# Performance work log

Hardware: AMD Instinct MI355X
Metric: run time of the kernel (lower is better)

## Reference

```python
import jax, jax.numpy as jnp
import numpy as np

B, S, HID = 1, 4096, 2048
H, HKV, D = 16, 4, 128
BLOCK = 32          # dllm_block_length
EPS = 1e-6
SCALE = D ** -0.5


def setup_inputs() -> dict:
    key = jax.random.key(0)
    ks = jax.random.split(key, 4)
    hidden_states = jax.random.normal(ks[0], (B, S, HID), dtype=jnp.float32)
    # RoPE tables (interleaved-half convention), shape [S, D]
    inv_freq = 1.0 / (10000.0 ** (np.arange(0, D, 2, dtype=np.float32) / D))
    t = np.arange(S, dtype=np.float32)
    freqs = np.outer(t, inv_freq)                      # [S, D/2]
    emb = np.concatenate([freqs, freqs], axis=-1)      # [S, D]
    cos = jnp.asarray(np.cos(emb), dtype=jnp.float32)
    sin = jnp.asarray(np.sin(emb), dtype=jnp.float32)
    w_qkv = jax.random.normal(ks[1], (HID, (H + 2 * HKV) * D), dtype=jnp.float32) * (HID ** -0.5)
    w_o = jax.random.normal(ks[2], (H * D, HID), dtype=jnp.float32) * ((H * D) ** -0.5)
    q_norm_w = jnp.ones((D,), dtype=jnp.float32)
    k_norm_w = jnp.ones((D,), dtype=jnp.float32)
    return {"hidden_states": hidden_states, "cos": cos, "sin": sin,
            "w_qkv": w_qkv, "q_norm_w": q_norm_w, "k_norm_w": k_norm_w, "w_o": w_o}


def _rms_norm(x, w):
    var = jnp.mean(jnp.square(x), axis=-1, keepdims=True)
    return x * jax.lax.rsqrt(var + EPS) * w


def _rotate_half(x):
    x1, x2 = jnp.split(x, 2, axis=-1)
    return jnp.concatenate([-x2, x1], axis=-1)


def reference(hidden_states, cos, sin, w_qkv, q_norm_w, k_norm_w, w_o):
    b, s, _ = hidden_states.shape
    qkv = hidden_states @ w_qkv                                   # [B,S,(H+2Hkv)*D]
    q = qkv[..., : H * D].reshape(b, s, H, D)
    k = qkv[..., H * D: (H + HKV) * D].reshape(b, s, HKV, D)
    v = qkv[..., (H + HKV) * D:].reshape(b, s, HKV, D)
    # per-head RMSNorm on q/k (use_qk_norm)
    q = _rms_norm(q, q_norm_w)
    k = _rms_norm(k, k_norm_w)
    # RoPE
    c = cos[None, :, None, :]
    sn = sin[None, :, None, :]
    q = q * c + _rotate_half(q) * sn
    k = k * c + _rotate_half(k) * sn
    # GQA: repeat kv heads
    rep = H // HKV
    k = jnp.repeat(k, rep, axis=2)                                # [B,S,H,D]
    v = jnp.repeat(v, rep, axis=2)
    scores = jnp.einsum("bshd,bthd->bhst", q, k) * SCALE          # [B,H,S,S]
    # block-diffusion mask: bidirectional within a dllm block, causal across blocks
    blk = jnp.arange(s) // BLOCK
    allowed = blk[None, :] <= blk[:, None]                        # [S,S]
    scores = jnp.where(allowed[None, None], scores, jnp.finfo(scores.dtype).min)
    attn = jax.nn.softmax(scores, axis=-1)
    out = jnp.einsum("bhst,bthd->bshd", attn, v).reshape(b, s, H * D)
    return out @ w_o
```

## Files before the change

kernel.cpp:

```cpp
#include <hip/hip_runtime.h>
#include <cstdint>

typedef __bf16 bf16;
typedef __attribute__((ext_vector_type(4))) __bf16 bf16x4;
typedef __attribute__((ext_vector_type(8))) __bf16 bf16x8;
typedef __attribute__((ext_vector_type(4))) float f32x4;

#define MFMA16(a, b, c) __builtin_amdgcn_mfma_f32_16x16x32_bf16((a), (b), (c), 0, 0, 0)

static __device__ __forceinline__ void gload16(const void* g, void* l) {
  __builtin_amdgcn_global_load_lds(
      (const __attribute__((address_space(1))) void*)g,
      (__attribute__((address_space(3))) void*)l, 16, 0, 0);
}

#define SWZ128(r, k) ((r) * 128 + ((k) ^ (((r) & 7) << 3)))
#define SWZP(r, k)   ((r) * 64  + ((k) ^ (((r) & 7) << 3)))
#define SWZV(r, k)   ((r) * 64  + ((k) ^ (((r) & 7) << 3)))

__global__ __launch_bounds__(256) void k_convert(const float* __restrict__ in,
                                                 bf16* __restrict__ out, int n4) {
  int i = blockIdx.x * blockDim.x + threadIdx.x;
  if (i >= n4) return;
  float4 v = *(const float4*)&in[(size_t)i * 4];
  bf16x4 o;
  o[0] = (bf16)v.x; o[1] = (bf16)v.y; o[2] = (bf16)v.z; o[3] = (bf16)v.w;
  *(bf16x4*)&out[(size_t)i * 4] = o;
}

__global__ void k_transpose(const float* __restrict__ in, bf16* __restrict__ out,
                            int R, int C) {
  __shared__ float tile[32][33];
  int bx = blockIdx.x, by = blockIdx.y;
  int tx = threadIdx.x, ty = threadIdx.y;
#pragma unroll
  for (int i = ty; i < 32; i += 8)
    tile[i][tx] = in[(size_t)(by * 32 + i) * C + bx * 32 + tx];
  __syncthreads();
#pragma unroll
  for (int i = ty; i < 32; i += 8)
    out[(size_t)(bx * 32 + i) * R + by * 32 + tx] = (bf16)tile[tx][i];
}

__global__ void k_vtrans(const bf16* __restrict__ qkv, bf16* __restrict__ vtg) {
  __shared__ bf16 tile[32][33];
  int s0 = blockIdx.x * 32, d0 = blockIdx.y * 32, hk = blockIdx.z;
  int tx = threadIdx.x, ty = threadIdx.y;
#pragma unroll
  for (int i = ty; i < 32; i += 8)
    tile[i][tx] = qkv[(size_t)(s0 + i) * 3072 + 2560 + hk * 128 + d0 + tx];
  __syncthreads();
#pragma unroll
  for (int i = ty; i < 32; i += 8)
    vtg[(size_t)hk * 524288 + (size_t)(d0 + i) * 4096 + s0 + tx] = tile[tx][i];
}

template <typename OutT>
__global__ __launch_bounds__(256) void k_gemm(const bf16* __restrict__ A,
                                              const bf16* __restrict__ BT,
                                              OutT* __restrict__ C, int M, int N, int K) {
  __shared__ bf16 As[128 * 32];
  __shared__ bf16 Bs[128 * 32];
  const int tid = threadIdx.x;
  const int wv = tid >> 6, lane = tid & 63;
  const int lr = lane & 15, lg = lane >> 4;
  const int wm = (wv >> 1) * 64, wn = (wv & 1) * 64;
  const int bm = blockIdx.x, bn = blockIdx.y;
  const size_t baseA = (size_t)bm * 128 * K;
  const size_t baseB = (size_t)bn * 128 * K;
  f32x4 acc[4][4] = {};
  for (int kt = 0; kt < K; kt += 32) {
    __syncthreads();
#pragma unroll
    for (int inst = 0; inst < 2; ++inst) {
      int ch = inst * 256 + tid;
      int row = ch >> 2, ko = (ch & 3) * 8;
      gload16(A + baseA + (size_t)row * K + kt + ko, &As[(size_t)(inst * 256 + wv * 64) * 8]);
      gload16(BT + baseB + (size_t)row * K + kt + ko, &Bs[(size_t)(inst * 256 + wv * 64) * 8]);
    }
    __syncthreads();
    bf16x8 af[4], bfr[4];
#pragma unroll
    for (int mi = 0; mi < 4; ++mi) af[mi] = *(const bf16x8*)&As[(wm + mi * 16 + lr) * 32 + lg * 8];
#pragma unroll
    for (int nj = 0; nj < 4; ++nj) bfr[nj] = *(const bf16x8*)&Bs[(wn + nj * 16 + lr) * 32 + lg * 8];
#pragma unroll
    for (int mi = 0; mi < 4; ++mi)
#pragma unroll
      for (int nj = 0; nj < 4; ++nj)
        acc[mi][nj] = MFMA16(af[mi], bfr[nj], acc[mi][nj]);
  }
#pragma unroll
  for (int mi = 0; mi < 4; ++mi)
#pragma unroll
    for (int nj = 0; nj < 4; ++nj)
#pragma unroll
      for (int j = 0; j < 4; ++j) {
        int r = bm * 128 + wm + mi * 16 + lg * 4 + j;
        int c = bn * 128 + wn + nj * 16 + lr;
        C[(size_t)r * N + c] = (OutT)acc[mi][nj][j];
      }
}

__global__ __launch_bounds__(256) void k_rmsrope(bf16* __restrict__ qkv,
                                                 const float* __restrict__ cosb,
                                                 const float* __restrict__ sinb,
                                                 const float* __restrict__ qw,
                                                 const float* __restrict__ kw) {
  int row = blockIdx.x * 4 + (threadIdx.x >> 6);
  int lane = threadIdx.x & 63;
  int s = row / 20, hd = row % 20;
  bool isq = hd < 16;
  int col = isq ? hd * 128 : 2048 + (hd - 16) * 128;
  bf16* p = qkv + (size_t)s * 3072 + col;
  float x1 = (float)p[lane], x2 = (float)p[lane + 64];
  float ss = x1 * x1 + x2 * x2;
#pragma unroll
  for (int m = 32; m; m >>= 1) ss += __shfl_xor(ss, m);
  float r = rsqrtf(ss * (1.0f / 128.0f) + 1e-6f);
  const float* w = isq ? qw : kw;
  float y1 = x1 * r * w[lane], y2 = x2 * r * w[lane + 64];
  float c1 = cosb[s * 128 + lane], c2 = cosb[s * 128 + lane + 64];
  float s1 = sinb[s * 128 + lane], s2 = sinb[s * 128 + lane + 64];
  p[lane] = (bf16)(y1 * c1 - y2 * s1);
  p[lane + 64] = (bf16)(y2 * c2 + y1 * s2);
}

__global__ __launch_bounds__(512, 2) void k_attn(const bf16* __restrict__ qkv,
                                                 const bf16* __restrict__ vtg,
                                                 bf16* __restrict__ out,
                                                 bf16* __restrict__ pO,
                                                 float2* __restrict__ pml) {
  __shared__ bf16 Ks[64 * 128];
  __shared__ bf16 Pl[128 * 64];
  __shared__ bf16 Vt[128 * 64];
  const int tid = threadIdx.x;
  const int wv = tid >> 6, lane = tid & 63;
  const int lr = lane & 15, lg = lane >> 4;
  const int b = blockIdx.x;
  int h, qt, kb0, kb1, tile = 0, half = 0;
  bool split;
  if (b < 256) {
    h = b & 15; qt = b >> 4; kb0 = 0; kb1 = 2 * qt + 2; split = false;
  } else {
    half = (b >= 512);
    int u = b - (half ? 512 : 256);
    h = u & 15; qt = 31 - (u >> 4);
    tile = h * 16 + (qt - 16);
    const int nh = qt + 1;
    kb0 = half ? nh : 0;
    kb1 = half ? 2 * qt + 2 : nh;
    split = true;
  }
  const int q0 = qt * 128;
  const int hk = h >> 2;
  const int wq = wv * 16;
  const float K2 = 0.12751744f;

  const int chK0 = tid, chK1 = 512 + tid;
  const int rowK0 = chK0 >> 4, rowK1 = chK1 >> 4;
  const int doffK0 = ((chK0 & 15) * 8) ^ ((rowK0 & 7) << 3);
  const int doffK1 = ((chK1 & 15) * 8) ^ ((rowK1 & 7) << 3);
  const int drow0 = chK0 >> 3, drow1 = chK1 >> 3;
  const int koffV0 = ((chK0 & 7) * 8) ^ ((drow0 & 7) << 3);
  const int koffV1 = ((chK1 & 7) * 8) ^ ((drow1 & 7) << 3);
  const bf16* kp0 = qkv + 2048 + hk * 128 + doffK0 + (size_t)(kb0 * 64 + rowK0) * 3072;
  const bf16* kp1 = qkv + 2048 + hk * 128 + doffK1 + (size_t)(kb0 * 64 + rowK1) * 3072;
  const bf16* vp0 = vtg + (size_t)hk * 524288 + (size_t)drow0 * 4096 + koffV0 + kb0 * 64;
  const bf16* vp1 = vtg + (size_t)hk * 524288 + (size_t)drow1 * 4096 + koffV1 + kb0 * 64;

  bf16x8 qf[4];
  {
    const bf16* qrow = qkv + (size_t)(q0 + wq + lr) * 3072 + h * 128 + lg * 8;
#pragma unroll
    for (int kk = 0; kk < 4; ++kk) {
      bf16x8 v = *(const bf16x8*)(qrow + kk * 32);
#pragma unroll
      for (int i = 0; i < 8; ++i) v[i] = (bf16)((float)v[i] * K2);
      qf[kk] = v;
    }
  }

  f32x4 oacc[8] = {};
  float mst = -1e30f, lst = 0.f;
  const int lim = (wq + lr) | 31;

  for (int kb = kb0; kb < kb1; ++kb) {
    __syncthreads();
    gload16(kp0, &Ks[(size_t)(wv * 64) * 8]);
    gload16(kp1, &Ks[(size_t)(512 + wv * 64) * 8]);
    gload16(vp0, &Vt[(size_t)(wv * 64) * 8]);
    gload16(vp1, &Vt[(size_t)(512 + wv * 64) * 8]);
    kp0 += 64 * 3072; kp1 += 64 * 3072; vp0 += 64; vp1 += 64;
    __syncthreads();

    f32x4 sacc[4] = {};
#pragma unroll
    for (int kk = 0; kk < 4; ++kk) {
      bf16x8 bk[4];
#pragma unroll
      for (int a = 0; a < 4; ++a)
        bk[a] = *(const bf16x8*)&Ks[SWZ128(a * 16 + lr, kk * 32 + lg * 8)];
#pragma unroll
      for (int a = 0; a < 4; ++a)
        sacc[a] = MFMA16(bk[a], qf[kk], sacc[a]);
    }

    float rm = -1e30f;
    if (kb >= 2 * qt) {
      const int koff2 = (kb - 2 * qt) * 64;
#pragma unroll
      for (int a = 0; a < 4; ++a)
#pragma unroll
        for (int j = 0; j < 4; ++j) {
          float sv = sacc[a][j];
          if (koff2 + a * 16 + lg * 4 + j > lim) sv = -1e30f;
          sacc[a][j] = sv;
          rm = fmaxf(rm, sv);
        }
    } else {
#pragma unroll
      for (int a = 0; a < 4; ++a)
#pragma unroll
        for (int j = 0; j < 4; ++j) rm = fmaxf(rm, sacc[a][j]);
    }
    rm = fmaxf(rm, __shfl_xor(rm, 16));
    rm = fmaxf(rm, __shfl_xor(rm, 32));
    if (__any(rm - mst > 8.0f)) {
      float mnew = fmaxf(mst, rm);
      float al = exp2f(mst - mnew);
      mst = mnew;
      lst *= al;
      float alo[4];
#pragma unroll
      for (int j = 0; j < 4; ++j) alo[j] = __shfl(al, lg * 4 + j);
#pragma unroll
      for (int dj = 0; dj < 8; ++dj)
#pragma unroll
        for (int j = 0; j < 4; ++j) oacc[dj][j] *= alo[j];
    }
    float rs = 0.f;
#pragma unroll
    for (int a = 0; a < 4; ++a) {
      bf16x4 pw;
#pragma unroll
      for (int j = 0; j < 4; ++j) {
        float p = exp2f(sacc[a][j] - mst);
        rs += p;
        pw[j] = (bf16)p;
      }
      *(bf16x4*)&Pl[SWZP(wq + lr, a * 16 + lg * 4)] = pw;
    }
    rs += __shfl_xor(rs, 16);
    rs += __shfl_xor(rs, 32);
    lst += rs;

#pragma unroll
    for (int kk = 0; kk < 2; ++kk) {
      bf16x8 ap = *(const bf16x8*)&Pl[SWZP(wq + lr, kk * 32 + lg * 8)];
#pragma unroll
      for (int dj = 0; dj < 8; ++dj) {
        bf16x8 bv = *(const bf16x8*)&Vt[SWZV(dj * 16 + lr, kk * 32 + lg * 8)];
        oacc[dj] = MFMA16(ap, bv, oacc[dj]);
      }
    }
  }

  float lrec = 1.0f / lst;
  float linv[4];
#pragma unroll
  for (int j = 0; j < 4; ++j) linv[j] = __shfl(lrec, lg * 4 + j);
  if (!split) {
#pragma unroll
    for (int dj = 0; dj < 8; ++dj)
#pragma unroll
      for (int j = 0; j < 4; ++j) {
        int srow = q0 + wq + lg * 4 + j;
        int d = dj * 16 + lr;
        out[(size_t)srow * 2048 + h * 128 + d] = (bf16)(oacc[dj][j] * linv[j]);
      }
  } else {
    if (lg == 0) pml[((size_t)half * 256 + tile) * 128 + wq + lr] = make_float2(mst, lst);
    bf16* pb = pO + (((size_t)half * 256 + tile) * 128) * 128;
#pragma unroll
    for (int dj = 0; dj < 8; ++dj)
#pragma unroll
      for (int j = 0; j < 4; ++j) {
        int row = wq + lg * 4 + j;
        int d = dj * 16 + lr;
        pb[(size_t)row * 128 + d] = (bf16)(oacc[dj][j] * linv[j]);
      }
  }
}

__global__ __launch_bounds__(256) void k_comb(const bf16* __restrict__ pO,
                                              const float2* __restrict__ pml,
                                              bf16* __restrict__ attno) {
  const int tile = blockIdx.x;
  const int h = tile >> 4, qt = 16 + (tile & 15);
  const int t = threadIdx.x;
  const int r = blockIdx.y * 32 + (t >> 3);
  const int d0 = (t & 7) * 16;
  float2 m0 = pml[(size_t)tile * 128 + r];
  float2 m1 = pml[(size_t)(256 + tile) * 128 + r];
  float mm = fmaxf(m0.x, m1.x);
  float w0 = m0.y * exp2f(m0.x - mm);
  float w1 = m1.y * exp2f(m1.x - mm);
  float inv = 1.0f / (w0 + w1);
  w0 *= inv; w1 *= inv;
  const bf16* p0 = pO + ((size_t)tile * 128 + r) * 128 + d0;
  const bf16* p1 = pO + ((size_t)(256 + tile) * 128 + r) * 128 + d0;
  bf16* o = attno + (size_t)(qt * 128 + r) * 2048 + h * 128 + d0;
#pragma unroll
  for (int v = 0; v < 2; ++v) {
    bf16x8 a = *(const bf16x8*)(p0 + v * 8);
    bf16x8 c = *(const bf16x8*)(p1 + v * 8);
    bf16x8 ov;
#pragma unroll
    for (int i = 0; i < 8; ++i) ov[i] = (bf16)((float)a[i] * w0 + (float)c[i] * w1);
    *(bf16x8*)(o + v * 8) = ov;
  }
}

extern "C" void kernel_launch(void* const* d_in, const int* in_sizes, int n_in,
                              void* d_out, int out_size, void* d_ws, size_t ws_size,
                              hipStream_t stream) {
  const float* hs = (const float*)d_in[0];
  const float* cosb = (const float*)d_in[1];
  const float* sinb = (const float*)d_in[2];
  const float* w_qkv = (const float*)d_in[3];
  const float* qw = (const float*)d_in[4];
  const float* kw = (const float*)d_in[5];
  const float* w_o = (const float*)d_in[6];
  float* out = (float*)d_out;

  char* ws = (char*)d_ws;
  bf16* qkv   = (bf16*)(ws);
  bf16* hsb   = (bf16*)(ws + 25165824);
  bf16* wqkvT = (bf16*)(ws + 41943040);
  bf16* woT   = (bf16*)(ws + 41943040);
  bf16* attno = (bf16*)(ws + 25165824);
  bf16* vtg   = (bf16*)(ws + 54525952);
  bf16* pO    = (bf16*)(ws + 58720256);
  float2* pml = (float2*)(ws + 75497472);

  k_convert<<<8192, 256, 0, stream>>>(hs, hsb, 2097152);
  k_transpose<<<dim3(96, 64), dim3(32, 8), 0, stream>>>(w_qkv, wqkvT, 2048, 3072);
  k_gemm<bf16><<<dim3(32, 24), 256, 0, stream>>>(hsb, wqkvT, qkv, 4096, 3072, 2048);
  k_rmsrope<<<20480, 256, 0, stream>>>(qkv, cosb, sinb, qw, kw);
  k_vtrans<<<dim3(128, 4, 4), dim3(32, 8), 0, stream>>>(qkv, vtg);
  k_transpose<<<dim3(64, 64), dim3(32, 8), 0, stream>>>(w_o, woT, 2048, 2048);
  k_attn<<<768, 512, 0, stream>>>(qkv, vtg, attno, pO, pml);
  k_comb<<<dim3(256, 4), 256, 0, stream>>>(pO, pml, attno);
  k_gemm<float><<<dim3(32, 16), 256, 0, stream>>>(attno, woT, out, 4096, 2048, 2048);
}
```

Before: 292.3 us.

## Fuse per-head RMSNorm and RoPE into the QKV projection GEMM epilogue

Replaces the generic QKV GEMM plus separate RMSNorm/RoPE kernel with a dedicated GEMM whose 128-column tile equals one head. Warps now own full 128-wide rows, so the epilogue can reduce the sum of squares with lane shuffles, apply the norm weight and rotate-half RoPE, then write bf16 directly. This removes one kernel launch and a full read and write of the q/k activations. In exchange the tile shape changes to 32x128 per warp with 16 accumulators, and the epilogue issues scattered scalar cos/sin loads and stores, which may change register pressure and GEMM efficiency.

```diff
diff --git a/kernel.cpp b/kernel.cpp
--- a/kernel.cpp
+++ b/kernel.cpp
@@ -102,28 +102,89 @@
       }
 }
 
-__global__ __launch_bounds__(256) void k_rmsrope(bf16* __restrict__ qkv,
-                                                 const float* __restrict__ cosb,
-                                                 const float* __restrict__ sinb,
-                                                 const float* __restrict__ qw,
-                                                 const float* __restrict__ kw) {
-  int row = blockIdx.x * 4 + (threadIdx.x >> 6);
-  int lane = threadIdx.x & 63;
-  int s = row / 20, hd = row % 20;
-  bool isq = hd < 16;
-  int col = isq ? hd * 128 : 2048 + (hd - 16) * 128;
-  bf16* p = qkv + (size_t)s * 3072 + col;
-  float x1 = (float)p[lane], x2 = (float)p[lane + 64];
-  float ss = x1 * x1 + x2 * x2;
-#pragma unroll
-  for (int m = 32; m; m >>= 1) ss += __shfl_xor(ss, m);
-  float r = rsqrtf(ss * (1.0f / 128.0f) + 1e-6f);
-  const float* w = isq ? qw : kw;
-  float y1 = x1 * r * w[lane], y2 = x2 * r * w[lane + 64];
-  float c1 = cosb[s * 128 + lane], c2 = cosb[s * 128 + lane + 64];
-  float s1 = sinb[s * 128 + lane], s2 = sinb[s * 128 + lane + 64];
-  p[lane] = (bf16)(y1 * c1 - y2 * s1);
-  p[lane + 64] = (bf16)(y2 * c2 + y1 * s2);
+__global__ __launch_bounds__(256) void k_gemm_qkv(const bf16* __restrict__ A,
+                                                  const bf16* __restrict__ BT,
+                                                  bf16* __restrict__ qkv,
+                                                  const float* __restrict__ cosb,
+                                                  const float* __restrict__ sinb,
+                                                  const float* __restrict__ qw,
+                                                  const float* __restrict__ kw) {
+  __shared__ bf16 As[128 * 32];
+  __shared__ bf16 Bs[128 * 32];
+  const int K = 2048;
+  const int tid = threadIdx.x;
+  const int wv = tid >> 6, lane = tid & 63;
+  const int lr = lane & 15, lg = lane >> 4;
+  const int wm = wv * 32;
+  const int bm = blockIdx.x, bn = blockIdx.y;
+  const size_t baseA = (size_t)bm * 128 * K;
+  const size_t baseB = (size_t)bn * 128 * K;
+  f32x4 acc[2][8] = {};
+  for (int kt = 0; kt < K; kt += 32) {
+    __syncthreads();
+#pragma unroll
+    for (int inst = 0; inst < 2; ++inst) {
+      int ch = inst * 256 + tid;
+      int row = ch >> 2, ko = (ch & 3) * 8;
+      gload16(A + baseA + (size_t)row * K + kt + ko, &As[(size_t)(inst * 256 + wv * 64) * 8]);
+      gload16(BT + baseB + (size_t)row * K + kt + ko, &Bs[(size_t)(inst * 256 + wv * 64) * 8]);
+    }
+    __syncthreads();
+    bf16x8 af[2], bfr[8];
+#pragma unroll
+    for (int mi = 0; mi < 2; ++mi) af[mi] = *(const bf16x8*)&As[(wm + mi * 16 + lr) * 32 + lg * 8];
+#pragma unroll
+    for (int nj = 0; nj < 8; ++nj) bfr[nj] = *(const bf16x8*)&Bs[(nj * 16 + lr) * 32 + lg * 8];
+#pragma unroll
+    for (int mi = 0; mi < 2; ++mi)
+#pragma unroll
+      for (int nj = 0; nj < 8; ++nj)
+        acc[mi][nj] = MFMA16(af[mi], bfr[nj], acc[mi][nj]);
+  }
+
+  if (bn < 20) {
+    const float* wt = (bn < 16) ? qw : kw;
+    float wreg[8];
+#pragma unroll
+    for (int nj = 0; nj < 8; ++nj) wreg[nj] = wt[nj * 16 + lr];
+#pragma unroll
+    for (int mi = 0; mi < 2; ++mi)
+#pragma unroll
+      for (int j = 0; j < 4; ++j) {
+        float s2 = 0.f;
+#pragma unroll
+        for (int nj = 0; nj < 8; ++nj) s2 += acc[mi][nj][j] * acc[mi][nj][j];
+        s2 += __shfl_xor(s2, 1);
+        s2 += __shfl_xor(s2, 2);
+        s2 += __shfl_xor(s2, 4);
+        s2 += __shfl_xor(s2, 8);
+        float rinv = rsqrtf(s2 * (1.0f / 128.0f) + 1e-6f);
+        int s = bm * 128 + wm + mi * 16 + lg * 4 + j;
+        const float* cr = cosb + (size_t)s * 128;
+        const float* sr = sinb + (size_t)s * 128;
+        float y[8];
+#pragma unroll
+        for (int nj = 0; nj < 8; ++nj) y[nj] = acc[mi][nj][j] * rinv * wreg[nj];
+        bf16* orow = qkv + (size_t)s * 3072 + bn * 128;
+#pragma unroll
+        for (int nj = 0; nj < 8; ++nj) {
+          int d = nj * 16 + lr;
+          float rot = (nj < 4) ? -y[nj + 4] : y[nj - 4];
+          orow[d] = (bf16)(y[nj] * cr[d] + rot * sr[d]);
+        }
+      }
+  } else {
+#pragma unroll
+    for (int mi = 0; mi < 2; ++mi)
+#pragma unroll
+      for (int nj = 0; nj < 8; ++nj)
+#pragma unroll
+        for (int j = 0; j < 4; ++j) {
+          int r = bm * 128 + wm + mi * 16 + lg * 4 + j;
+          int c = bn * 128 + nj * 16 + lr;
+          qkv[(size_t)r * 3072 + c] = (bf16)acc[mi][nj][j];
+        }
+  }
 }
 
 __global__ __launch_bounds__(512, 2) void k_attn(const bf16* __restrict__ qkv,
@@ -346,8 +407,7 @@
 
   k_convert<<<8192, 256, 0, stream>>>(hs, hsb, 2097152);
   k_transpose<<<dim3(96, 64), dim3(32, 8), 0, stream>>>(w_qkv, wqkvT, 2048, 3072);
-  k_gemm<bf16><<<dim3(32, 24), 256, 0, stream>>>(hsb, wqkvT, qkv, 4096, 3072, 2048);
-  k_rmsrope<<<20480, 256, 0, stream>>>(qkv, cosb, sinb, qw, kw);
+  k_gemm_qkv<<<dim3(32, 24), 256, 0, stream>>>(hsb, wqkvT, qkv, cosb, sinb, qw, kw);
   k_vtrans<<<dim3(128, 4, 4), dim3(32, 8), 0, stream>>>(qkv, vtg);
   k_transpose<<<dim3(64, 64), dim3(32, 8), 0, stream>>>(w_o, woT, 2048, 2048);
   k_attn<<<768, 512, 0, stream>>>(qkv, vtg, attno, pO, pml);
```

Result: no change. 297.8 us (+1.9%).
